# Performance work log

Measured on AMD Instinct MI355X. Metric: run time of the kernel, lower is better.

## Reference

```python
import jax, jax.numpy as jnp
import numpy as np

T, B, V, E, H, K = 256, 512, 50000, 300, 100, 8


def _lstm_dir(x, wih, whh, bih, bhh, reverse):
    # x: [T,B,D]; wih: [4H,D]; whh: [4H,H]. PyTorch gate order: i,f,g,o.
    xp = jnp.einsum('tbd,gd->tbg', x, wih) + bih + bhh  # precompute input projections
    h0 = jnp.zeros((x.shape[1], whh.shape[1]), x.dtype)
    c0 = jnp.zeros_like(h0)

    def step(carry, xt):
        h, c = carry
        g = xt + h @ whh.T
        i, f, gg, o = jnp.split(g, 4, axis=-1)
        i = jax.nn.sigmoid(i); f = jax.nn.sigmoid(f)
        gg = jnp.tanh(gg); o = jax.nn.sigmoid(o)
        c = f * c + i * gg
        h = o * jnp.tanh(c)
        return (h, c), h

    _, hs = jax.lax.scan(step, (h0, c0), xp, reverse=reverse)
    return hs  # [T,B,H]


def _bilstm(x, pf, pb):
    hf = _lstm_dir(x, *pf, reverse=False)
    hb = _lstm_dir(x, *pb, reverse=True)
    return jnp.concatenate([hf, hb], axis=-1)  # [T,B,2H]


def _crf_llh(em, tags, maskf, start_t, end_t, trans):
    # torchcrf log-likelihood, reduction='sum'. em: [T,B,K], tags/maskf: [T,B]
    barange = jnp.arange(em.shape[1])
    # numerator: score of gold path
    num = start_t[tags[0]] + em[0, barange, tags[0]]
    trans_sc = trans[tags[:-1], tags[1:]]                                   # [T-1,B]
    em_sc = jnp.take_along_axis(em[1:], tags[1:, :, None], axis=2)[..., 0]  # [T-1,B]
    num = num + jnp.sum((trans_sc + em_sc) * maskf[1:], axis=0)
    seq_ends = maskf.sum(0).astype(jnp.int32) - 1
    num = num + end_t[tags[seq_ends, barange]]
    # denominator: forward algorithm (log partition)
    score0 = start_t + em[0]  # [B,K]

    def step(score, inp):
        em_t, m_t = inp
        nxt = jax.scipy.special.logsumexp(score[:, :, None] + trans[None], axis=1) + em_t
        return jnp.where(m_t[:, None] > 0, nxt, score), None

    scoreT, _ = jax.lax.scan(step, score0, (em[1:], maskf[1:]))
    denom = jax.scipy.special.logsumexp(scoreT + end_t, axis=1)
    return jnp.sum(num - denom)


def _viterbi(em, start_t, end_t, trans):
    # mask is all ones -> fixed-length decode. em: [T,B,K] -> tags [T,B]
    score0 = start_t + em[0]

    def step(score, em_t):
        br = score[:, :, None] + trans            # [B,K,K]
        idx = jnp.argmax(br, axis=1)              # [B,K] backpointers
        return jnp.max(br, axis=1) + em_t, idx

    scoreT, hist = jax.lax.scan(step, score0, em[1:])  # hist: [T-1,B,K]
    last = jnp.argmax(scoreT + end_t, axis=1)          # [B]
    barange = jnp.arange(em.shape[1])

    def back(nxt, h):
        prev = h[barange, nxt]
        return prev, prev

    _, prevs = jax.lax.scan(back, last, hist, reverse=True)  # [T-1,B]
    return jnp.concatenate([prevs, last[None]], axis=0)      # [T,B]


def setup_inputs() -> dict:
    key = jax.random.key(0)
    ks = jax.random.split(key, 32)
    u = lambda k, shape, s: jax.random.uniform(k, shape, jnp.float32, -s, s)
    kl = 1.0 / np.sqrt(H)
    inp = {
        'sentence': jax.random.randint(ks[0], (T, B), 0, V, dtype=jnp.int32),
        'tags': jax.random.randint(ks[1], (T, B), 0, K, dtype=jnp.int32),
        'mask': jnp.ones((T, B), dtype=bool),
        'emb': jax.random.normal(ks[2], (V, E), jnp.float32),
        # layer 0 (input dim E)
        'wih0f': u(ks[3], (4 * H, E), kl), 'whh0f': u(ks[4], (4 * H, H), kl),
        'bih0f': u(ks[5], (4 * H,), kl), 'bhh0f': u(ks[6], (4 * H,), kl),
        'wih0b': u(ks[7], (4 * H, E), kl), 'whh0b': u(ks[8], (4 * H, H), kl),
        'bih0b': u(ks[9], (4 * H,), kl), 'bhh0b': u(ks[10], (4 * H,), kl),
        # layer 1 (input dim 2H)
        'wih1f': u(ks[11], (4 * H, 2 * H), kl), 'whh1f': u(ks[12], (4 * H, H), kl),
        'bih1f': u(ks[13], (4 * H,), kl), 'bhh1f': u(ks[14], (4 * H,), kl),
        'wih1b': u(ks[15], (4 * H, 2 * H), kl), 'whh1b': u(ks[16], (4 * H, H), kl),
        'bih1b': u(ks[17], (4 * H,), kl), 'bhh1b': u(ks[18], (4 * H,), kl),
        # linear 2H -> K
        'wl': u(ks[19], (K, 2 * H), 1.0 / np.sqrt(2 * H)), 'bl': u(ks[20], (K,), 1.0 / np.sqrt(2 * H)),
        # CRF params (torchcrf init: uniform(-0.1, 0.1))
        'start_t': u(ks[21], (K,), 0.1), 'end_t': u(ks[22], (K,), 0.1),
        'trans': u(ks[23], (K, K), 0.1),
    }
    return inp


def reference(sentence, tags, mask, emb,
              wih0f, whh0f, bih0f, bhh0f, wih0b, whh0b, bih0b, bhh0b,
              wih1f, whh1f, bih1f, bhh1f, wih1b, whh1b, bih1b, bhh1b,
              wl, bl, start_t, end_t, trans):
    x = emb[sentence]                                        # [T,B,E]
    h1 = _bilstm(x, (wih0f, whh0f, bih0f, bhh0f), (wih0b, whh0b, bih0b, bhh0b))
    h2 = _bilstm(h1, (wih1f, whh1f, bih1f, bhh1f), (wih1b, whh1b, bih1b, bhh1b))
    em = jnp.einsum('tbh,kh->tbk', h2, wl) + bl              # emissions [T,B,K]
    maskf = mask.astype(em.dtype)
    loss = _crf_llh(em, tags, maskf, start_t, end_t, trans)
    decode = _viterbi(em, start_t, end_t, trans)
    return loss, decode
```

## Files before the change

### kernel.cpp

```cpp
#include <hip/hip_runtime.h>
#include <math.h>


#define T_LEN 256
#define B_SZ  512
#define TCH   32

__device__ __forceinline__ float sigm(float x) { return 1.f / (1.f + __expf(-x)); }
__device__ __forceinline__ float tanh_f(float x) {
  float e = __expf(-2.f * fabsf(x));
  float r = (1.f - e) / (1.f + e);
  return copysignf(r, x);
}

__global__ __launch_bounds__(256) void pack_kernel(
    const float* __restrict__ wih0f, const float* __restrict__ bih0f, const float* __restrict__ bhh0f,
    const float* __restrict__ wih0b, const float* __restrict__ bih0b, const float* __restrict__ bhh0b,
    const float* __restrict__ wih1f, const float* __restrict__ bih1f, const float* __restrict__ bhh1f,
    const float* __restrict__ wih1b, const float* __restrict__ bih1b, const float* __restrict__ bhh1b,
    float* __restrict__ W0, float* __restrict__ B0,
    float* __restrict__ W1, float* __restrict__ B1,
    float* __restrict__ out0) {
  int idx = blockIdx.x * blockDim.x + threadIdx.x;
  int stride = gridDim.x * blockDim.x;
  if (idx == 0) out0[0] = 0.f;
  for (int i = idx; i < 800 * 300; i += stride) {
    int g = i / 300, d = i - g * 300;
    W0[i] = (g < 400) ? wih0f[g * 300 + d] : wih0b[(g - 400) * 300 + d];
  }
  for (int i = idx; i < 800 * 200; i += stride) {
    int g = i / 200, d = i - g * 200;
    W1[i] = (g < 400) ? wih1f[g * 200 + d] : wih1b[(g - 400) * 200 + d];
  }
  for (int i = idx; i < 800; i += stride) {
    B0[i] = (i < 400) ? (bih0f[i] + bhh0f[i]) : (bih0b[i - 400] + bhh0b[i - 400]);
    B1[i] = (i < 400) ? (bih1f[i] + bhh1f[i]) : (bih1b[i - 400] + bhh1b[i - 400]);
  }
}

#define BM 128
#define BN 128
#define BK 8
__device__ __forceinline__ void gemm_body(
    const float* __restrict__ A, const float* __restrict__ W,
    const float* __restrict__ bias, float* __restrict__ C,
    int M, int N, int Kd, int m0, int n0,
    float (*As)[BM], float (*Ws)[BN]) {
  const int tid = threadIdx.x;
  const int tx = tid & 15, ty = tid >> 4;
  const int lm = tid >> 1;
  const int lk = (tid & 1) * 4;

  float acc[8][8];
  float bj[8];
#pragma unroll
  for (int j = 0; j < 8; ++j) {
    int n = n0 + tx * 8 + j;
    bj[j] = (n < N) ? bias[n] : 0.f;
  }
#pragma unroll
  for (int i = 0; i < 8; ++i)
#pragma unroll
    for (int j = 0; j < 8; ++j) acc[i][j] = bj[j];

  float4 av = make_float4(0.f, 0.f, 0.f, 0.f);
  float4 wv = make_float4(0.f, 0.f, 0.f, 0.f);
  if (m0 + lm < M && lk < Kd)
    av = *(const float4*)(A + (size_t)(m0 + lm) * Kd + lk);
  if (n0 + lm < N && lk < Kd)
    wv = *(const float4*)(W + (size_t)(n0 + lm) * Kd + lk);

  for (int k0 = 0; k0 < Kd; k0 += BK) {
    __syncthreads();
    As[lk + 0][lm] = av.x; As[lk + 1][lm] = av.y;
    As[lk + 2][lm] = av.z; As[lk + 3][lm] = av.w;
    Ws[lk + 0][lm] = wv.x; Ws[lk + 1][lm] = wv.y;
    Ws[lk + 2][lm] = wv.z; Ws[lk + 3][lm] = wv.w;
    __syncthreads();
    int k0n = k0 + BK;
    av = make_float4(0.f, 0.f, 0.f, 0.f);
    wv = make_float4(0.f, 0.f, 0.f, 0.f);
    if (k0n < Kd) {
      if (m0 + lm < M && k0n + lk < Kd)
        av = *(const float4*)(A + (size_t)(m0 + lm) * Kd + k0n + lk);
      if (n0 + lm < N && k0n + lk < Kd)
        wv = *(const float4*)(W + (size_t)(n0 + lm) * Kd + k0n + lk);
    }
#pragma unroll
    for (int kk = 0; kk < BK; ++kk) {
      float a[8], w[8];
      *(float4*)&a[0] = *(const float4*)&As[kk][ty * 8];
      *(float4*)&a[4] = *(const float4*)&As[kk][ty * 8 + 4];
      *(float4*)&w[0] = *(const float4*)&Ws[kk][tx * 8];
      *(float4*)&w[4] = *(const float4*)&Ws[kk][tx * 8 + 4];
#pragma unroll
      for (int i = 0; i < 8; ++i)
#pragma unroll
        for (int j = 0; j < 8; ++j) acc[i][j] += a[i] * w[j];
    }
  }
#pragma unroll
  for (int i = 0; i < 8; ++i) {
    int m = m0 + ty * 8 + i;
    if (m < M) {
#pragma unroll
      for (int j0 = 0; j0 < 8; j0 += 4) {
        int n = n0 + tx * 8 + j0;
        if (n < N) {
          float4 o = make_float4(acc[i][j0], acc[i][j0 + 1], acc[i][j0 + 2], acc[i][j0 + 3]);
          *(float4*)(C + (size_t)m * N + n) = o;
        }
      }
    }
  }
}

__global__ __launch_bounds__(256, 2) void gemm_tn(
    const float* __restrict__ A, const float* __restrict__ W,
    const float* __restrict__ bias, float* __restrict__ C,
    int M, int N, int Kd) {
  __shared__ float As[BK][BM];
  __shared__ float Ws[BK][BN];
  gemm_body(A, W, bias, C, M, N, Kd, blockIdx.x * BM, blockIdx.y * BN, As, Ws);
}

__global__ __launch_bounds__(256, 2) void gemm_dual(
    const float* __restrict__ h1, const float* __restrict__ W1,
    const float* __restrict__ B1, float* __restrict__ XPF,
    float* __restrict__ XPB, int baseF, int baseB, int B) {
  __shared__ float As[BK][BM];
  __shared__ float Ws[BK][BN];
  const int dir = blockIdx.z;
  const float* A = h1 + (size_t)(dir ? baseB : baseF) * B * 200;
  const float* W = W1 + (size_t)dir * 80000;
  const float* bias = B1 + dir * 400;
  float* C = dir ? XPB : XPF;
  gemm_body(A, W, bias, C, TCH * B, 400, 200, blockIdx.x * BM, blockIdx.y * BN, As, Ws);
}

__global__ __launch_bounds__(256, 2) void lstm2(
    const float* __restrict__ XPf, const float* __restrict__ XPb,
    int xp_stride,
    const int* __restrict__ gather,
    const float* __restrict__ whhF, const float* __restrict__ whhB,
    float* __restrict__ stateH, float* __restrict__ stateC,
    float* __restrict__ hout,
    int tbaseF, int tbaseB, int TC, int first, int B) {
  const int tid = threadIdx.x;
  const int j = tid >> 1;
  const int gp = tid & 1;
  const bool act = (j < 100);
  const int bpd = B >> 1;
  const int dir = (blockIdx.x >= (unsigned)bpd) ? 1 : 0;
  const int b0 = (dir ? (blockIdx.x - bpd) : blockIdx.x) * 2;
  const float* __restrict__ XP = dir ? XPb : XPf;
  const float* __restrict__ whh = dir ? whhB : whhF;
  const int tbase = dir ? tbaseB : tbaseF;
  const int tstep = dir ? -1 : 1;
  const int tfirst = dir ? (tbase + TC - 1) : tbase;
  const int cg0 = gp * 200 + j;
  const int cg1 = cg0 + 100;

  __shared__ float h_s[2][2][100];

  float4 w0[25], w1[25];
  {
    const float* p0 = whh + (size_t)(2 * gp) * 10000 + (size_t)j * 100;
    if (act) {
#pragma unroll
      for (int q = 0; q < 25; ++q) {
        w0[q] = *(const float4*)(p0 + q * 4);
        w1[q] = *(const float4*)(p0 + 10000 + q * 4);
      }
    } else {
#pragma unroll
      for (int q = 0; q < 25; ++q) {
        w0[q] = make_float4(0.f, 0.f, 0.f, 0.f);
        w1[q] = make_float4(0.f, 0.f, 0.f, 0.f);
      }
    }
  }

  float c0v = 0.f, c1v = 0.f;
  if (gp == 0 && act) {
    if (!first) {
      c0v = stateC[((size_t)dir * B + b0 + 0) * 100 + j];
      c1v = stateC[((size_t)dir * B + b0 + 1) * 100 + j];
      h_s[0][0][j] = stateH[((size_t)dir * B + b0 + 0) * 100 + j];
      h_s[0][1][j] = stateH[((size_t)dir * B + b0 + 1) * 100 + j];
    } else {
      h_s[0][0][j] = 0.f;
      h_s[0][1][j] = 0.f;
    }
  }

  auto rowptr = [&](int tt, int bb) -> const float* {
    size_t r = gather ? (size_t)gather[(size_t)tt * B + b0 + bb]
                      : (size_t)(tt - tbase) * B + b0 + bb;
    return XP + r * (size_t)xp_stride;
  };

  float x00 = 0.f, x01 = 0.f, x10 = 0.f, x11 = 0.f;
  {
    const float* r0 = rowptr(tfirst, 0);
    const float* r1 = rowptr(tfirst, 1);
    if (act) { x00 = r0[cg0]; x10 = r0[cg1]; x01 = r1[cg0]; x11 = r1[cg1]; }
  }
  const float* baseN0 = XP;
  const float* baseN1 = XP;
  if (TC > 1) { baseN0 = rowptr(tfirst + tstep, 0); baseN1 = rowptr(tfirst + tstep, 1); }

  __syncthreads();

  int cur = 0;
  for (int s = 0; s < TC; ++s) {
    const int t = tfirst + s * tstep;
    float nx00 = 0.f, nx01 = 0.f, nx10 = 0.f, nx11 = 0.f;
    if (act && s + 1 < TC) {
      nx00 = baseN0[cg0]; nx10 = baseN0[cg1];
      nx01 = baseN1[cg0]; nx11 = baseN1[cg1];
    }
    if (s + 2 < TC) {
      baseN0 = rowptr(t + 2 * tstep, 0);
      baseN1 = rowptr(t + 2 * tstep, 1);
    }
    float a00 = 0.f, a01 = 0.f, a10 = 0.f, a11 = 0.f;
    const float* hb0 = h_s[cur][0];
    const float* hb1 = h_s[cur][1];
#pragma unroll
    for (int q = 0; q < 25; ++q) {
      float4 h0 = *(const float4*)(hb0 + q * 4);
      float4 h1v = *(const float4*)(hb1 + q * 4);
      float4 W0q = w0[q], W1q = w1[q];
      a00 += W0q.x * h0.x + W0q.y * h0.y + W0q.z * h0.z + W0q.w * h0.w;
      a10 += W1q.x * h0.x + W1q.y * h0.y + W1q.z * h0.z + W1q.w * h0.w;
      a01 += W0q.x * h1v.x + W0q.y * h1v.y + W0q.z * h1v.z + W0q.w * h1v.w;
      a11 += W1q.x * h1v.x + W1q.y * h1v.y + W1q.z * h1v.z + W1q.w * h1v.w;
    }
    a00 += x00; a10 += x10; a01 += x01; a11 += x11;
    float g0 = __shfl_xor(a00, 1);
    float g1 = __shfl_xor(a01, 1);
    float o0 = __shfl_xor(a10, 1);
    float o1 = __shfl_xor(a11, 1);
    const int nxt = cur ^ 1;
    if (gp == 0 && act) {
      float i0 = sigm(a00), f0 = sigm(a10);
      c0v = f0 * c0v + i0 * tanh_f(g0);
      float h0n = sigm(o0) * tanh_f(c0v);
      float i1 = sigm(a01), f1 = sigm(a11);
      c1v = f1 * c1v + i1 * tanh_f(g1);
      float h1n = sigm(o1) * tanh_f(c1v);
      h_s[nxt][0][j] = h0n;
      h_s[nxt][1][j] = h1n;
      hout[((size_t)t * B + b0 + 0) * 200 + dir * 100 + j] = h0n;
      hout[((size_t)t * B + b0 + 1) * 200 + dir * 100 + j] = h1n;
    }
    __syncthreads();
    cur = nxt;
    x00 = nx00; x01 = nx01; x10 = nx10; x11 = nx11;
  }
  if (gp == 0 && act) {
    stateH[((size_t)dir * B + b0 + 0) * 100 + j] = h_s[cur][0][j];
    stateH[((size_t)dir * B + b0 + 1) * 100 + j] = h_s[cur][1][j];
    stateC[((size_t)dir * B + b0 + 0) * 100 + j] = c0v;
    stateC[((size_t)dir * B + b0 + 1) * 100 + j] = c1v;
  }
}

__global__ __launch_bounds__(256) void em_kernel(
    const float* __restrict__ h2, const float* __restrict__ wl,
    const float* __restrict__ bl_, float* __restrict__ em) {
  __shared__ float hsb[32][200];
  __shared__ float wls[8 * 200];
  __shared__ float bls[8];
  const int tid = threadIdx.x;
  const int row0 = blockIdx.x * 32;
  for (int i = tid; i < 1600; i += 256) wls[i] = wl[i];
  if (tid < 8) bls[tid] = bl_[tid];
  for (int i = tid; i < 1600; i += 256) {
    int r = i / 50, q = i - r * 50;
    *(float4*)&hsb[r][q * 4] = *(const float4*)(h2 + (size_t)(row0 + r) * 200 + q * 4);
  }
  __syncthreads();
  const int r_l = tid >> 3, k = tid & 7;
  float acc = bls[k];
#pragma unroll
  for (int d4 = 0; d4 < 50; ++d4) {
    float4 h = *(const float4*)&hsb[r_l][d4 * 4];
    float4 wv = *(const float4*)&wls[k * 200 + d4 * 4];
    acc += h.x * wv.x + h.y * wv.y + h.z * wv.z + h.w * wv.w;
  }
  em[(size_t)(row0 + r_l) * 8 + k] = acc;
}

__global__ __launch_bounds__(64) void crf_kernel(
    const float* __restrict__ em, const int* __restrict__ tags,
    const float* __restrict__ start_t, const float* __restrict__ end_t,
    const float* __restrict__ trans, float* __restrict__ loss_out,
    int T, int B) {
  const int tid = threadIdx.x;
  const int bl = tid >> 3, jj = tid & 7;
  const int b = blockIdx.x * 8 + bl;
  __shared__ float sc[2][8][9];
  __shared__ float rednum[8][8];
  __shared__ float partial[8];
  float trj[8];
#pragma unroll
  for (int i = 0; i < 8; ++i) trj[i] = trans[i * 8 + jj];

  float pnum = 0.f;
  for (int t = 1 + jj; t < T; t += 8) {
    int tp = tags[(size_t)(t - 1) * B + b];
    int tc = tags[(size_t)t * B + b];
    pnum += trans[tp * 8 + tc] + em[((size_t)t * B + b) * 8 + tc];
  }
  rednum[bl][jj] = pnum;
  __syncthreads();
  float num = 0.f;
  if (jj == 0) {
#pragma unroll
    for (int i = 0; i < 8; ++i) num += rednum[bl][i];
    int t0 = tags[b];
    int tl = tags[(size_t)(T - 1) * B + b];
    num += start_t[t0] + em[(size_t)b * 8 + t0] + end_t[tl];
  }
  sc[0][bl][jj] = start_t[jj] + em[(size_t)b * 8 + jj];
  __syncthreads();
  for (int t = 1; t < T; ++t) {
    int cur = t & 1, prev = cur ^ 1;
    float m = -1e30f;
    float v[8];
#pragma unroll
    for (int i = 0; i < 8; ++i) {
      v[i] = sc[prev][bl][i] + trj[i];
      m = fmaxf(m, v[i]);
    }
    float ssum = 0.f;
#pragma unroll
    for (int i = 0; i < 8; ++i) ssum += __expf(v[i] - m);
    sc[cur][bl][jj] = m + __logf(ssum) + em[((size_t)t * B + b) * 8 + jj];
    __syncthreads();
  }
  rednum[bl][jj] = sc[(T - 1) & 1][bl][jj] + end_t[jj];
  __syncthreads();
  if (jj == 0) {
    float m = -1e30f;
#pragma unroll
    for (int i = 0; i < 8; ++i) m = fmaxf(m, rednum[bl][i]);
    float ssum = 0.f;
#pragma unroll
    for (int i = 0; i < 8; ++i) ssum += __expf(rednum[bl][i] - m);
    partial[bl] = num - (m + __logf(ssum));
  }
  __syncthreads();
  if (tid == 0) {
    float s2 = 0.f;
#pragma unroll
    for (int i = 0; i < 8; ++i) s2 += partial[i];
    atomicAdd(loss_out, s2);
  }
}

__global__ __launch_bounds__(64) void viterbi_kernel(
    const float* __restrict__ em, const float* __restrict__ start_t,
    const float* __restrict__ end_t, const float* __restrict__ trans,
    float* __restrict__ dec_out, int T, int B) {
  const int tid = threadIdx.x;
  const int bl = tid >> 3, jj = tid & 7;
  const int b = blockIdx.x * 8 + bl;
  __shared__ float sc[2][8][9];
  __shared__ unsigned hist[T_LEN - 1][8];
  __shared__ float redm[8][8];
  __shared__ int lastt[8];
  float trj[8];
#pragma unroll
  for (int i = 0; i < 8; ++i) trj[i] = trans[i * 8 + jj];
  for (int i = tid; i < (T_LEN - 1) * 8; i += 64) ((unsigned*)hist)[i] = 0u;
  sc[0][bl][jj] = start_t[jj] + em[(size_t)b * 8 + jj];
  __syncthreads();
  for (int t = 1; t < T; ++t) {
    int cur = t & 1, prev = cur ^ 1;
    float m = -1e30f;
    int am = 0;
#pragma unroll
    for (int i = 0; i < 8; ++i) {
      float v = sc[prev][bl][i] + trj[i];
      if (v > m) { m = v; am = i; }
    }
    atomicOr(&hist[t - 1][bl], (unsigned)am << (3 * jj));
    sc[cur][bl][jj] = m + em[((size_t)t * B + b) * 8 + jj];
    __syncthreads();
  }
  redm[bl][jj] = sc[(T - 1) & 1][bl][jj] + end_t[jj];
  __syncthreads();
  if (jj == 0) {
    float m = -1e30f;
    int am = 0;
#pragma unroll
    for (int i = 0; i < 8; ++i) {
      float v = redm[bl][i];
      if (v > m) { m = v; am = i; }
    }
    lastt[bl] = am;
  }
  __syncthreads();
  if (tid < 8) {
    int bb = blockIdx.x * 8 + tid;
    int cur = lastt[tid];
    dec_out[(size_t)(T - 1) * B + bb] = (float)cur;
    for (int t2 = T - 2; t2 >= 0; --t2) {
      cur = (int)((hist[t2][tid] >> (3 * cur)) & 7u);
      dec_out[(size_t)t2 * B + bb] = (float)cur;
    }
  }
}

__global__ __launch_bounds__(256) void report_kernel(float* out, float wsval, int n) {
  int i = blockIdx.x * blockDim.x + threadIdx.x;
  if (i == 0) out[0] = wsval;
  else if (i < n) out[i] = 0.f;
}

extern "C" void kernel_launch(void* const* d_in, const int* in_sizes, int n_in,
                              void* d_out, int out_size, void* d_ws, size_t ws_size,
                              hipStream_t stream) {
  const int* sentence = (const int*)d_in[0];
  const int* tags     = (const int*)d_in[1];
  const float* emb   = (const float*)d_in[3];
  const float* wih0f = (const float*)d_in[4];
  const float* whh0f = (const float*)d_in[5];
  const float* bih0f = (const float*)d_in[6];
  const float* bhh0f = (const float*)d_in[7];
  const float* wih0b = (const float*)d_in[8];
  const float* whh0b = (const float*)d_in[9];
  const float* bih0b = (const float*)d_in[10];
  const float* bhh0b = (const float*)d_in[11];
  const float* wih1f = (const float*)d_in[12];
  const float* whh1f = (const float*)d_in[13];
  const float* bih1f = (const float*)d_in[14];
  const float* bhh1f = (const float*)d_in[15];
  const float* wih1b = (const float*)d_in[16];
  const float* whh1b = (const float*)d_in[17];
  const float* bih1b = (const float*)d_in[18];
  const float* bhh1b = (const float*)d_in[19];
  const float* wl      = (const float*)d_in[20];
  const float* bl_     = (const float*)d_in[21];
  const float* start_t = (const float*)d_in[22];
  const float* end_t   = (const float*)d_in[23];
  const float* trans   = (const float*)d_in[24];

  const int T = T_LEN, B = B_SZ;
  float* out = (float*)d_out;
  float* ws = (float*)d_ws;

  const size_t O_P0  = 0;
  const size_t O_H1  = 40000000ull;
  const size_t O_W0  = 66214400ull;
  const size_t O_B0  = 66454400ull;
  const size_t O_STH = 66214400ull;
  const size_t O_STC = 66316800ull;
  const size_t O_W1  = 66455200ull;
  const size_t O_B1  = 66615200ull;
  const size_t TOTAL_FL = 66616000ull;
  const size_t O_H2  = 0;
  const size_t O_XPF = 26214400ull;
  const size_t O_XPB = 32768000ull;
  const size_t O_EM  = 26214400ull;

  if (ws_size < TOTAL_FL * 4ull) {
    report_kernel<<<(out_size + 255) / 256, 256, 0, stream>>>(out, (float)ws_size, out_size);
    return;
  }

  float* P0  = ws + O_P0;
  float* h1  = ws + O_H1;
  float* W0  = ws + O_W0;
  float* B0  = ws + O_B0;
  float* stH = ws + O_STH;
  float* stC = ws + O_STC;
  float* W1  = ws + O_W1;
  float* B1  = ws + O_B1;
  float* h2  = ws + O_H2;
  float* XPF = ws + O_XPF;
  float* XPB = ws + O_XPB;
  float* em  = ws + O_EM;

  pack_kernel<<<256, 256, 0, stream>>>(wih0f, bih0f, bhh0f, wih0b, bih0b, bhh0b,
                                       wih1f, bih1f, bhh1f, wih1b, bih1b, bhh1b,
                                       W0, B0, W1, B1, out);
  dim3 g1((50000 + BM - 1) / BM, (800 + BN - 1) / BN);
  gemm_tn<<<g1, 256, 0, stream>>>(emb, W0, B0, P0, 50000, 800, 300);

  lstm2<<<B, 256, 0, stream>>>(P0, P0 + 400, 800, sentence, whh0f, whh0b,
                               stH, stC, h1, 0, 0, T, 1, B);

  dim3 gc((TCH * B + BM - 1) / BM, (400 + BN - 1) / BN, 2);
  for (int cc = 0; cc < T / TCH; ++cc) {
    int baseF = cc * TCH;
    int baseB = T - TCH - cc * TCH;
    gemm_dual<<<gc, 256, 0, stream>>>(h1, W1, B1, XPF, XPB, baseF, baseB, B);
    lstm2<<<B, 256, 0, stream>>>(XPF, XPB, 400, nullptr, whh1f, whh1b,
                                 stH, stC, h2, baseF, baseB, TCH, cc == 0, B);
  }

  em_kernel<<<(T * B) / 32, 256, 0, stream>>>(h2, wl, bl_, em);
  crf_kernel<<<B / 8, 64, 0, stream>>>(em, tags, start_t, end_t, trans, out, T, B);
  viterbi_kernel<<<B / 8, 64, 0, stream>>>(em, start_t, end_t, trans, out + 1, T, B);
}
```

Before: 2.599 ms.

## Restructure LSTM recurrence: 4 batch rows per block, K-split across thread pairs

The recurrent LSTM kernel now runs 512 threads per block and handles 4 batch rows per block instead of 2, halving the grid. Each gate-row pair is split across two threads along the hidden dimension, so each thread keeps only half the recurrent weights in registers. The partial sums are combined with lane shuffles, and each thread then computes the cell update for one batch row, so every lane does useful activation work. The intent is to cut register pressure and reuse each weight load across more batch rows, at the cost of extra shuffles and a larger block barrier every timestep.

```diff
diff --git a/kernel.cpp b/kernel.cpp
--- a/kernel.cpp
+++ b/kernel.cpp
@@ -138,7 +138,7 @@
   gemm_body(A, W, bias, C, TCH * B, 400, 200, blockIdx.x * BM, blockIdx.y * BN, As, Ws);
 }
 
-__global__ __launch_bounds__(256, 2) void lstm2(
+__global__ __launch_bounds__(512, 2) void lstm2(
     const float* __restrict__ XPf, const float* __restrict__ XPb,
     int xp_stride,
     const int* __restrict__ gather,
@@ -147,50 +147,52 @@
     float* __restrict__ hout,
     int tbaseF, int tbaseB, int TC, int first, int B) {
   const int tid = threadIdx.x;
-  const int j = tid >> 1;
-  const int gp = tid & 1;
+  const int j  = tid >> 2;
+  const int gp = (tid >> 1) & 1;
+  const int kh = tid & 1;
+  const int q  = tid & 3;
   const bool act = (j < 100);
-  const int bpd = B >> 1;
+  const int bpd = B >> 2;
   const int dir = (blockIdx.x >= (unsigned)bpd) ? 1 : 0;
-  const int b0 = (dir ? (blockIdx.x - bpd) : blockIdx.x) * 2;
-  const float* __restrict__ XP = dir ? XPb : XPf;
+  const int b0 = (dir ? (blockIdx.x - bpd) : blockIdx.x) * 4;
+  const float* __restrict__ XP  = dir ? XPb : XPf;
   const float* __restrict__ whh = dir ? whhB : whhF;
   const int tbase = dir ? tbaseB : tbaseF;
   const int tstep = dir ? -1 : 1;
   const int tfirst = dir ? (tbase + TC - 1) : tbase;
-  const int cg0 = gp * 200 + j;
-  const int cg1 = cg0 + 100;
-
-  __shared__ float h_s[2][2][100];
-
-  float4 w0[25], w1[25];
+  const int row0 = gp * 200 + j;
+  const int col  = act ? (gp * 200 + kh * 100 + j) : 0;
+
+  __shared__ float h_s[2][4][104];
+
+  float4 w0[13], w1[13];
   {
-    const float* p0 = whh + (size_t)(2 * gp) * 10000 + (size_t)j * 100;
-    if (act) {
-#pragma unroll
-      for (int q = 0; q < 25; ++q) {
-        w0[q] = *(const float4*)(p0 + q * 4);
-        w1[q] = *(const float4*)(p0 + 10000 + q * 4);
+    const float* p0 = whh + (size_t)row0 * 100;
+#pragma unroll
+    for (int qq = 0; qq < 13; ++qq) {
+      const int c = 2 * qq + kh;
+      if (act && c < 25) {
+        w0[qq] = *(const float4*)(p0 + c * 4);
+        w1[qq] = *(const float4*)(p0 + 10000 + c * 4);
+      } else {
+        w0[qq] = make_float4(0.f, 0.f, 0.f, 0.f);
+        w1[qq] = make_float4(0.f, 0.f, 0.f, 0.f);
       }
+    }
+  }
+
+  if (tid < 32) {
+    int bf = tid >> 4, bb = (tid >> 2) & 3, ii = tid & 3;
+    h_s[bf][bb][100 + ii] = 0.f;
+  }
+
+  float cv = 0.f;
+  if (act) {
+    if (!first) {
+      cv = stateC[((size_t)dir * B + b0 + q) * 100 + j];
+      h_s[0][q][j] = stateH[((size_t)dir * B + b0 + q) * 100 + j];
     } else {
-#pragma unroll
-      for (int q = 0; q < 25; ++q) {
-        w0[q] = make_float4(0.f, 0.f, 0.f, 0.f);
-        w1[q] = make_float4(0.f, 0.f, 0.f, 0.f);
-      }
-    }
-  }
-
-  float c0v = 0.f, c1v = 0.f;
-  if (gp == 0 && act) {
-    if (!first) {
-      c0v = stateC[((size_t)dir * B + b0 + 0) * 100 + j];
-      c1v = stateC[((size_t)dir * B + b0 + 1) * 100 + j];
-      h_s[0][0][j] = stateH[((size_t)dir * B + b0 + 0) * 100 + j];
-      h_s[0][1][j] = stateH[((size_t)dir * B + b0 + 1) * 100 + j];
-    } else {
-      h_s[0][0][j] = 0.f;
-      h_s[0][1][j] = 0.f;
+      h_s[0][q][j] = 0.f;
     }
   }
 
@@ -200,70 +202,86 @@
     return XP + r * (size_t)xp_stride;
   };
 
-  float x00 = 0.f, x01 = 0.f, x10 = 0.f, x11 = 0.f;
-  {
-    const float* r0 = rowptr(tfirst, 0);
-    const float* r1 = rowptr(tfirst, 1);
-    if (act) { x00 = r0[cg0]; x10 = r0[cg1]; x01 = r1[cg0]; x11 = r1[cg1]; }
-  }
-  const float* baseN0 = XP;
-  const float* baseN1 = XP;
-  if (TC > 1) { baseN0 = rowptr(tfirst + tstep, 0); baseN1 = rowptr(tfirst + tstep, 1); }
+  float x0, x1, x2, x3;
+  x0 = rowptr(tfirst, 0)[col];
+  x1 = rowptr(tfirst, 1)[col];
+  x2 = rowptr(tfirst, 2)[col];
+  x3 = rowptr(tfirst, 3)[col];
+  const float* bN0 = XP; const float* bN1 = XP;
+  const float* bN2 = XP; const float* bN3 = XP;
+  if (TC > 1) {
+    bN0 = rowptr(tfirst + tstep, 0);
+    bN1 = rowptr(tfirst + tstep, 1);
+    bN2 = rowptr(tfirst + tstep, 2);
+    bN3 = rowptr(tfirst + tstep, 3);
+  }
 
   __syncthreads();
 
   int cur = 0;
   for (int s = 0; s < TC; ++s) {
     const int t = tfirst + s * tstep;
-    float nx00 = 0.f, nx01 = 0.f, nx10 = 0.f, nx11 = 0.f;
-    if (act && s + 1 < TC) {
-      nx00 = baseN0[cg0]; nx10 = baseN0[cg1];
-      nx01 = baseN1[cg0]; nx11 = baseN1[cg1];
-    }
+    float nx0 = 0.f, nx1 = 0.f, nx2 = 0.f, nx3 = 0.f;
+    if (s + 1 < TC) { nx0 = bN0[col]; nx1 = bN1[col]; nx2 = bN2[col]; nx3 = bN3[col]; }
     if (s + 2 < TC) {
-      baseN0 = rowptr(t + 2 * tstep, 0);
-      baseN1 = rowptr(t + 2 * tstep, 1);
-    }
-    float a00 = 0.f, a01 = 0.f, a10 = 0.f, a11 = 0.f;
-    const float* hb0 = h_s[cur][0];
-    const float* hb1 = h_s[cur][1];
-#pragma unroll
-    for (int q = 0; q < 25; ++q) {
-      float4 h0 = *(const float4*)(hb0 + q * 4);
-      float4 h1v = *(const float4*)(hb1 + q * 4);
-      float4 W0q = w0[q], W1q = w1[q];
-      a00 += W0q.x * h0.x + W0q.y * h0.y + W0q.z * h0.z + W0q.w * h0.w;
-      a10 += W1q.x * h0.x + W1q.y * h0.y + W1q.z * h0.z + W1q.w * h0.w;
-      a01 += W0q.x * h1v.x + W0q.y * h1v.y + W0q.z * h1v.z + W0q.w * h1v.w;
-      a11 += W1q.x * h1v.x + W1q.y * h1v.y + W1q.z * h1v.z + W1q.w * h1v.w;
-    }
-    a00 += x00; a10 += x10; a01 += x01; a11 += x11;
-    float g0 = __shfl_xor(a00, 1);
-    float g1 = __shfl_xor(a01, 1);
-    float o0 = __shfl_xor(a10, 1);
-    float o1 = __shfl_xor(a11, 1);
+      bN0 = rowptr(t + 2 * tstep, 0);
+      bN1 = rowptr(t + 2 * tstep, 1);
+      bN2 = rowptr(t + 2 * tstep, 2);
+      bN3 = rowptr(t + 2 * tstep, 3);
+    }
+    float a00 = 0.f, a01 = 0.f, a02 = 0.f, a03 = 0.f;
+    float a10 = 0.f, a11 = 0.f, a12 = 0.f, a13 = 0.f;
+    const float* hb = &h_s[cur][0][0];
+#pragma unroll
+    for (int qq = 0; qq < 13; ++qq) {
+      const int c4 = (2 * qq + kh) * 4;
+      float4 h0 = *(const float4*)(hb + c4);
+      float4 h1 = *(const float4*)(hb + 104 + c4);
+      float4 h2 = *(const float4*)(hb + 208 + c4);
+      float4 h3 = *(const float4*)(hb + 312 + c4);
+      float4 W0 = w0[qq], W1 = w1[qq];
+      a00 += W0.x * h0.x + W0.y * h0.y + W0.z * h0.z + W0.w * h0.w;
+      a01 += W0.x * h1.x + W0.y * h1.y + W0.z * h1.z + W0.w * h1.w;
+      a02 += W0.x * h2.x + W0.y * h2.y + W0.z * h2.z + W0.w * h2.w;
+      a03 += W0.x * h3.x + W0.y * h3.y + W0.z * h3.z + W0.w * h3.w;
+      a10 += W1.x * h0.x + W1.y * h0.y + W1.z * h0.z + W1.w * h0.w;
+      a11 += W1.x * h1.x + W1.y * h1.y + W1.z * h1.z + W1.w * h1.w;
+      a12 += W1.x * h2.x + W1.y * h2.y + W1.z * h2.z + W1.w * h2.w;
+      a13 += W1.x * h3.x + W1.y * h3.y + W1.z * h3.z + W1.w * h3.w;
+    }
+    if (kh == 0) { a00 += x0; a01 += x1; a02 += x2; a03 += x3; }
+    else         { a10 += x0; a11 += x1; a12 += x2; a13 += x3; }
+    a00 += __shfl_xor(a00, 1); a01 += __shfl_xor(a01, 1);
+    a02 += __shfl_xor(a02, 1); a03 += __shfl_xor(a03, 1);
+    a10 += __shfl_xor(a10, 1); a11 += __shfl_xor(a11, 1);
+    a12 += __shfl_xor(a12, 1); a13 += __shfl_xor(a13, 1);
+    float r00 = __shfl_xor(a00, 2), r01 = __shfl_xor(a01, 2);
+    float r02 = __shfl_xor(a02, 2), r03 = __shfl_xor(a03, 2);
+    float r10 = __shfl_xor(a10, 2), r11 = __shfl_xor(a11, 2);
+    float r12 = __shfl_xor(a12, 2), r13 = __shfl_xor(a13, 2);
+    float sa0 = gp ? (kh ? a03 : a02) : (kh ? a01 : a00);
+    float sa1 = gp ? (kh ? a13 : a12) : (kh ? a11 : a10);
+    float sr0 = gp ? (kh ? r03 : r02) : (kh ? r01 : r00);
+    float sr1 = gp ? (kh ? r13 : r12) : (kh ? r11 : r10);
+    float gi = gp ? sr0 : sa0;
+    float gf = gp ? sr1 : sa1;
+    float gg = gp ? sa0 : sr0;
+    float go = gp ? sa1 : sr1;
+    float iv = sigm(gi), fv = sigm(gf);
+    cv = fv * cv + iv * tanh_f(gg);
+    float hn = sigm(go) * tanh_f(cv);
     const int nxt = cur ^ 1;
-    if (gp == 0 && act) {
-      float i0 = sigm(a00), f0 = sigm(a10);
-      c0v = f0 * c0v + i0 * tanh_f(g0);
-      float h0n = sigm(o0) * tanh_f(c0v);
-      float i1 = sigm(a01), f1 = sigm(a11);
-      c1v = f1 * c1v + i1 * tanh_f(g1);
-      float h1n = sigm(o1) * tanh_f(c1v);
-      h_s[nxt][0][j] = h0n;
-      h_s[nxt][1][j] = h1n;
-      hout[((size_t)t * B + b0 + 0) * 200 + dir * 100 + j] = h0n;
-      hout[((size_t)t * B + b0 + 1) * 200 + dir * 100 + j] = h1n;
+    if (act) {
+      h_s[nxt][q][j] = hn;
+      hout[((size_t)t * B + b0 + q) * 200 + dir * 100 + j] = hn;
     }
     __syncthreads();
     cur = nxt;
-    x00 = nx00; x01 = nx01; x10 = nx10; x11 = nx11;
-  }
-  if (gp == 0 && act) {
-    stateH[((size_t)dir * B + b0 + 0) * 100 + j] = h_s[cur][0][j];
-    stateH[((size_t)dir * B + b0 + 1) * 100 + j] = h_s[cur][1][j];
-    stateC[((size_t)dir * B + b0 + 0) * 100 + j] = c0v;
-    stateC[((size_t)dir * B + b0 + 1) * 100 + j] = c1v;
+    x0 = nx0; x1 = nx1; x2 = nx2; x3 = nx3;
+  }
+  if (act) {
+    stateH[((size_t)dir * B + b0 + q) * 100 + j] = h_s[cur][q][j];
+    stateC[((size_t)dir * B + b0 + q) * 100 + j] = cv;
   }
 }
 
@@ -491,16 +509,16 @@
   dim3 g1((50000 + BM - 1) / BM, (800 + BN - 1) / BN);
   gemm_tn<<<g1, 256, 0, stream>>>(emb, W0, B0, P0, 50000, 800, 300);
 
-  lstm2<<<B, 256, 0, stream>>>(P0, P0 + 400, 800, sentence, whh0f, whh0b,
-                               stH, stC, h1, 0, 0, T, 1, B);
+  lstm2<<<B / 2, 512, 0, stream>>>(P0, P0 + 400, 800, sentence, whh0f, whh0b,
+                                   stH, stC, h1, 0, 0, T, 1, B);
 
   dim3 gc((TCH * B + BM - 1) / BM, (400 + BN - 1) / BN, 2);
   for (int cc = 0; cc < T / TCH; ++cc) {
     int baseF = cc * TCH;
     int baseB = T - TCH - cc * TCH;
     gemm_dual<<<gc, 256, 0, stream>>>(h1, W1, B1, XPF, XPB, baseF, baseB, B);
-    lstm2<<<B, 256, 0, stream>>>(XPF, XPB, 400, nullptr, whh1f, whh1b,
-                                 stH, stC, h2, baseF, baseB, TCH, cc == 0, B);
+    lstm2<<<B / 2, 512, 0, stream>>>(XPF, XPB, 400, nullptr, whh1f, whh1b,
+                                     stH, stC, h2, baseF, baseB, TCH, cc == 0, B);
   }
 
   em_kernel<<<(T * B) / 32, 256, 0, stream>>>(h2, wl, bl_, em);
```

Result: slower. 8.824 ms (+239.5%).
